# Kernel optimization log

Measured on AMD Instinct MI355X. Metric: run time of the kernel, lower is better.

The kernel has to match this reference:

```python
import jax, jax.numpy as jnp
import numpy as np

N_USERS = 100000
N_ITEMS = 50000
NNZ = 3000000  # user-item interactions; symmetric adjacency has 2*NNZ edges
D = 64
N_LAYERS = 3


def setup_inputs() -> dict:
    key = jax.random.key(0)
    k1, k2, k3 = jax.random.split(key, 3)
    N = N_USERS + N_ITEMS
    users = jax.random.randint(k1, (NNZ,), 0, N_USERS)
    items = jax.random.randint(k2, (NNZ,), 0, N_ITEMS) + N_USERS
    # symmetric bipartite adjacency: u->i and i->u edges
    row = jnp.concatenate([users, items]).astype(jnp.int32)
    col = jnp.concatenate([items, users]).astype(jnp.int32)
    # D^{-1/2} A D^{-1/2} normalization, matching (deg + 1e-7)^{-0.5}
    deg = jax.ops.segment_sum(jnp.ones(row.shape, dtype=jnp.float32), row, num_segments=N)
    dinv = jnp.power(deg + 1e-7, -0.5)
    vals = dinv[row] * dinv[col]
    in_embs = jax.random.normal(k3, (N, D), dtype=jnp.float32)
    return {"in_embs": in_embs, "row": row, "col": col, "vals": vals, "n_layers": N_LAYERS}


def reference(in_embs, row, col, vals, n_layers):
    N = in_embs.shape[0]
    # result = in_embs + sum_i [ x_i/(i+1) + x_i ]  (original appends both per layer)
    out = in_embs
    x = in_embs
    for i in range(n_layers):
        # SpMM: x <- A_norm @ x  via gather + segment scatter-add
        x = jax.ops.segment_sum(vals[:, None] * x[col], row, num_segments=N)
        # F.normalize(x, dim=-1) with torch's eps=1e-12 clamp
        x = x / jnp.maximum(jnp.linalg.norm(x, axis=-1, keepdims=True), 1e-12)
        out = out + x * (1.0 + 1.0 / (i + 1))
    return out
```

## Files before the change

kernel.cpp:

```cpp
#include <hip/hip_runtime.h>
#include <hip/hip_bf16.h>

#define D 64
#define BW 256
#define MAXK 1024
#define CHUNK 8192

typedef unsigned short u16;
typedef unsigned int u32;
typedef _Float16 half2_t __attribute__((ext_vector_type(2)));

__device__ __forceinline__ u16 f2h(float f) {
    union { _Float16 h; u16 u; } v; v.h = (_Float16)f; return v.u;
}
__device__ __forceinline__ float hlo(u32 u) {
    union { u32 x; half2_t h; } v; v.x = u; return (float)v.h.x;
}
__device__ __forceinline__ float hhi(u32 u) {
    union { u32 x; half2_t h; } v; v.x = u; return (float)v.h.y;
}
__device__ __forceinline__ float dot2lo(u32 u, float acc) {
    union { u32 x; half2_t h; } v; v.x = u;
    half2_t one = {(_Float16)1.0f, (_Float16)0.0f};
    return __builtin_amdgcn_fdot2(v.h, one, acc, false);
}
__device__ __forceinline__ float dot2hi(u32 u, float acc) {
    union { u32 x; half2_t h; } v; v.x = u;
    half2_t one = {(_Float16)0.0f, (_Float16)1.0f};
    return __builtin_amdgcn_fdot2(v.h, one, acc, false);
}


__global__ __launch_bounds__(256) void chunk_hist_kernel(
        const int* __restrict__ row, int* __restrict__ H,
        int E, int K, int nchunks) {
    __shared__ int h[MAXK];
    int ch = blockIdx.x;
    int cbeg = ch * CHUNK;
    int cend = min(cbeg + CHUNK, E);
    for (int i = threadIdx.x; i < K; i += 256) h[i] = 0;
    __syncthreads();
    for (int e = cbeg + threadIdx.x; e < cend; e += 256)
        atomicAdd(&h[__builtin_nontemporal_load(&row[e]) >> 8], 1);
    __syncthreads();
    for (int i = threadIdx.x; i < K; i += 256)
        H[(size_t)i * nchunks + ch] = h[i];
}


__global__ __launch_bounds__(256) void bucket_colscan_kernel(
        int* __restrict__ H, int* __restrict__ btot, int nchunks) {
    __shared__ int tmp[256];
    int b = blockIdx.x;
    int t = threadIdx.x;
    int* Hb = H + (size_t)b * nchunks;
    int cpt = (nchunks + 255) >> 8;
    int beg = min(t * cpt, nchunks), end = min(beg + cpt, nchunks);
    int s = 0;
    for (int i = beg; i < end; ++i) s += Hb[i];
    tmp[t] = s;
    __syncthreads();
    for (int d = 1; d < 256; d <<= 1) {
        int x = (t >= d) ? tmp[t - d] : 0;
        __syncthreads();
        tmp[t] += x;
        __syncthreads();
    }
    int run = tmp[t] - s;
    for (int i = beg; i < end; ++i) {
        int v = Hb[i];
        Hb[i] = run;
        run += v;
    }
    if (t == 255) btot[b] = tmp[255];
}


__global__ __launch_bounds__(1024) void bucket_scan_kernel(
        const int* __restrict__ btot, int* __restrict__ bbase, int K, int E) {
    __shared__ int tmp[1024];
    int t = threadIdx.x;
    int v = (t < K) ? btot[t] : 0;
    tmp[t] = v;
    __syncthreads();
    for (int d = 1; d < 1024; d <<= 1) {
        int x = (t >= d) ? tmp[t - d] : 0;
        __syncthreads();
        tmp[t] += x;
        __syncthreads();
    }
    if (t < K) bbase[t] = tmp[t] - v;
    if (t == 0) bbase[K] = E;
}


__global__ __launch_bounds__(256) void scatter_chunks_kernel(
        const int* __restrict__ row, const int* __restrict__ col,
        const int* __restrict__ H, const int* __restrict__ bbase,
        u32* __restrict__ pairs, int E, int K, int nchunks) {
    __shared__ int cur[MAXK];
    int ch = blockIdx.x;
    int cbeg = ch * CHUNK;
    int cend = min(cbeg + CHUNK, E);
    for (int i = threadIdx.x; i < K; i += 256)
        cur[i] = bbase[i] + H[(size_t)i * nchunks + ch];
    __syncthreads();
    for (int e = cbeg + threadIdx.x; e < cend; e += 256) {
        int r = __builtin_nontemporal_load(&row[e]);
        u32 c = (u32)__builtin_nontemporal_load(&col[e]);
        int p = atomicAdd(&cur[r >> 8], 1);
        pairs[p] = ((u32)(r & 255) << 18) | c;
    }
}


__global__ __launch_bounds__(256) void build_csr_kernel(
        const u32* __restrict__ pairs, const int* __restrict__ bbase,
        int* __restrict__ ptr, float* __restrict__ dinv,
        float* __restrict__ sdeg, int* __restrict__ ccol, int N, int K) {
    __shared__ int hd[BW];
    __shared__ int lp[BW];
    int k = blockIdx.x;
    int ebeg = bbase[k], eend = bbase[k + 1];
    int r0 = k << 8;
    int t = threadIdx.x;
    hd[t] = 0;
    __syncthreads();
    for (int e = ebeg + t; e < eend; e += 256)
        atomicAdd(&hd[pairs[e] >> 18], 1);
    __syncthreads();
    int v = hd[t];
    lp[t] = v;
    __syncthreads();
    for (int d = 1; d < 256; d <<= 1) {
        int x = (t >= d) ? lp[t - d] : 0;
        __syncthreads();
        lp[t] += x;
        __syncthreads();
    }
    int fillbase = ebeg + lp[t] - v;
    int r = r0 + t;
    if (r < N) {
        ptr[r] = fillbase;
        float f = (float)v + 1e-7f;
        float sq = sqrtf(f);
        dinv[r] = 1.0f / sq;
        sdeg[r] = sq;
    }
    hd[t] = fillbase;
    if (k == 0 && t == 0) ptr[N] = bbase[K];
    __syncthreads();
    for (int e = ebeg + t; e < eend; e += 256) {
        u32 pk = pairs[e];
        int pos = atomicAdd(&hd[pk >> 18], 1);
        ccol[pos] = (int)(pk & 0x3FFFFu);
    }
}

__global__ void scale_in_kernel(const float* __restrict__ in,
                                const float* __restrict__ dinv,
                                u16* __restrict__ y0, int npairs) {
    int p = blockIdx.x * blockDim.x + threadIdx.x;
    if (p >= npairs) return;
    float2 v = *reinterpret_cast<const float2*>(&in[(size_t)p * 2]);
    float dv = dinv[p >> 5];
    u32 up = (u32)f2h(v.x * dv) | ((u32)f2h(v.y * dv) << 16);
    *reinterpret_cast<u32*>(&y0[(size_t)p * 2]) = up;
}

template <bool FINAL>
__global__ __launch_bounds__(256) void layer_kernel(
        const u16* __restrict__ y_src,
        const int* __restrict__ ptr,
        const int* __restrict__ ccol,
        const float* __restrict__ dinv,
        const float* __restrict__ sdeg,
        u16* __restrict__ y_dst,
        const float* __restrict__ in_embs,
        const u16* __restrict__ y1,
        float* __restrict__ out,
        int rbeg, int rend) {
    int wid = (blockIdx.x * blockDim.x + threadIdx.x) >> 6;
    int lane = threadIdx.x & 63;
    int rh = lane >> 5;
    int b = (lane >> 3) & 3;
    int a = lane & 7;
    int r = rbeg + wid * 2 + rh;
    if (r >= rend) return;
    const size_t dimoff = (size_t)a * 8;

    int s = ptr[r], e = ptr[r + 1];
    float acc[8];
    #pragma unroll
    for (int i = 0; i < 8; ++i) acc[i] = 0.f;

#define ACCQ(q)                                            \
    do {                                                   \
        u32 qa_[4] = {(q).x, (q).y, (q).z, (q).w};         \
        _Pragma("unroll")                                  \
        for (int i_ = 0; i_ < 4; ++i_) {                   \
            acc[2 * i_]     = dot2lo(qa_[i_], acc[2 * i_]);     \
            acc[2 * i_ + 1] = dot2hi(qa_[i_], acc[2 * i_ + 1]); \
        }                                                  \
    } while (0)

    int j = s;
    #pragma unroll 2
    for (; j + 8 <= e; j += 8) {
        int c0 = __builtin_nontemporal_load(&ccol[j + b]);
        int c1 = __builtin_nontemporal_load(&ccol[j + 4 + b]);
        uint4 q0 = *reinterpret_cast<const uint4*>(&y_src[(size_t)c0 * D + dimoff]);
        uint4 q1 = *reinterpret_cast<const uint4*>(&y_src[(size_t)c1 * D + dimoff]);
        ACCQ(q0);
        ACCQ(q1);
    }
    if (j + 4 <= e) {
        int c = __builtin_nontemporal_load(&ccol[j + b]);
        uint4 q = *reinterpret_cast<const uint4*>(&y_src[(size_t)c * D + dimoff]);
        ACCQ(q);
        j += 4;
    }
    if (j + b < e) {
        int c = __builtin_nontemporal_load(&ccol[j + b]);
        uint4 q = *reinterpret_cast<const uint4*>(&y_src[(size_t)c * D + dimoff]);
        ACCQ(q);
    }
#undef ACCQ

    #pragma unroll
    for (int off = 8; off <= 16; off <<= 1) {
        #pragma unroll
        for (int i = 0; i < 8; ++i) acc[i] += __shfl_xor(acc[i], off);
    }

    float ss = 0.f;
    #pragma unroll
    for (int i = 0; i < 8; ++i) ss += acc[i] * acc[i];
    #pragma unroll
    for (int off = 1; off <= 4; off <<= 1) ss += __shfl_xor(ss, off);
    float inv = 1.0f / fmaxf(sqrtf(ss), 1e-12f);

    if (b == 0) {
        size_t idx = (size_t)r * D + dimoff;
        if (FINAL) {
            float sd = sdeg[r];
            float4 i0 = *reinterpret_cast<const float4*>(&in_embs[idx]);
            float4 i1 = *reinterpret_cast<const float4*>(&in_embs[idx + 4]);
            uint4 w1 = *reinterpret_cast<const uint4*>(&y1[idx]);
            uint4 w2 = *reinterpret_cast<const uint4*>(&y_src[idx]);
            u32 w1a[4] = {w1.x, w1.y, w1.z, w1.w};
            u32 w2a[4] = {w2.x, w2.y, w2.z, w2.w};
            float o[8];
            #pragma unroll
            for (int i = 0; i < 4; ++i) {
                o[2 * i]     = 2.0f * sd * hlo(w1a[i]) + 1.5f * sd * hlo(w2a[i])
                             + (4.0f / 3.0f) * acc[2 * i] * inv;
                o[2 * i + 1] = 2.0f * sd * hhi(w1a[i]) + 1.5f * sd * hhi(w2a[i])
                             + (4.0f / 3.0f) * acc[2 * i + 1] * inv;
            }
            float4 o0 = {o[0] + i0.x, o[1] + i0.y, o[2] + i0.z, o[3] + i0.w};
            float4 o1 = {o[4] + i1.x, o[5] + i1.y, o[6] + i1.z, o[7] + i1.w};
            *reinterpret_cast<float4*>(&out[idx])     = o0;
            *reinterpret_cast<float4*>(&out[idx + 4]) = o1;
        } else {
            float dv = dinv[r] * inv;
            uint4 w;
            w.x = (u32)f2h(acc[0] * dv) | ((u32)f2h(acc[1] * dv) << 16);
            w.y = (u32)f2h(acc[2] * dv) | ((u32)f2h(acc[3] * dv) << 16);
            w.z = (u32)f2h(acc[4] * dv) | ((u32)f2h(acc[5] * dv) << 16);
            w.w = (u32)f2h(acc[6] * dv) | ((u32)f2h(acc[7] * dv) << 16);
            *reinterpret_cast<uint4*>(&y_dst[idx]) = w;
        }
    }
}


__global__ void spmm_scatter_kernel(const float* __restrict__ x_src,
                                    const int* __restrict__ row,
                                    const int* __restrict__ col,
                                    const float* __restrict__ vals,
                                    float* __restrict__ x_dst, int E) {
    int gid = blockIdx.x * blockDim.x + threadIdx.x;
    int e = gid >> 6;
    int lane = threadIdx.x & 63;
    if (e >= E) return;
    float xv = x_src[(size_t)col[e] * D + lane];
    atomicAdd(&x_dst[(size_t)row[e] * D + lane], vals[e] * xv);
}

__global__ void norm_accum_kernel(float* __restrict__ x, float* __restrict__ out,
                                  float coef, int N) {
    int gid = blockIdx.x * blockDim.x + threadIdx.x;
    int rowi = gid >> 6;
    int lane = threadIdx.x & 63;
    if (rowi >= N) return;
    size_t idx = (size_t)rowi * D + lane;
    float v = x[idx];
    float s = v * v;
    #pragma unroll
    for (int off = 32; off >= 1; off >>= 1) s += __shfl_xor(s, off);
    float nv = v / fmaxf(sqrtf(s), 1e-12f);
    x[idx] = nv;
    out[idx] += coef * nv;
}

static inline size_t align256(size_t x) { return (x + 255) & ~(size_t)255; }

extern "C" void kernel_launch(void* const* d_in, const int* in_sizes, int n_in,
                              void* d_out, int out_size, void* d_ws, size_t ws_size,
                              hipStream_t stream) {
    const float* in_embs = (const float*)d_in[0];
    const int*   row     = (const int*)d_in[1];
    const int*   col     = (const int*)d_in[2];
    const float* vals    = (const float*)d_in[3];

    const int N = in_sizes[0] / D;
    const int E = in_sizes[1];

    float* out = (float*)d_out;

    const size_t embElems = (size_t)N * D;
    const size_t f16Bytes = embElems * sizeof(u16);
    const int K = (N + BW - 1) / BW;
    const int nchunks = (E + CHUNK - 1) / CHUNK;
    const size_t Hbytes = (size_t)K * nchunks * 4;

    size_t off = 0;
    const size_t o_ccol  = off; off += align256((size_t)E * 4);
    const size_t o_ptr   = off; off += align256(((size_t)N + 1) * 4);
    const size_t o_dinv  = off; off += align256((size_t)N * 4);
    const size_t o_sdeg  = off; off += align256((size_t)N * 4);
    const size_t o_btot  = off; off += align256((size_t)MAXK * 4);
    const size_t o_bbase = off; off += align256(((size_t)MAXK + 1) * 4);
    const size_t o_X     = off;
    const size_t xNeedA  = align256((size_t)E * 4) + align256(Hbytes);
    const size_t xNeedB  = 2 * align256(f16Bytes);
    const size_t xBytes  = (xNeedA > xNeedB) ? xNeedA : xNeedB;
    const size_t needed  = o_X + align256(xBytes);

    dim3 block(256);
    const int npairs = (int)(embElems / 2);
    dim3 pgrid((unsigned)((npairs + 255) / 256));

    if (ws_size >= needed && K <= MAXK) {
        char* wsb = (char*)d_ws;
        int*   ccol  = (int*)(wsb + o_ccol);
        int*   ptr   = (int*)(wsb + o_ptr);
        float* dinv  = (float*)(wsb + o_dinv);
        float* sdeg  = (float*)(wsb + o_sdeg);
        int*   btot  = (int*)(wsb + o_btot);
        int*   bbase = (int*)(wsb + o_bbase);
        u32*   pairs = (u32*)(wsb + o_X);
        int*   H     = (int*)(wsb + o_X + align256((size_t)E * 4));
        u16*   bufA  = (u16*)(wsb + o_X);
        u16*   bufB  = (u16*)(wsb + o_X + align256(f16Bytes));

        chunk_hist_kernel<<<dim3((unsigned)nchunks), block, 0, stream>>>(
            row, H, E, K, nchunks);
        bucket_colscan_kernel<<<dim3((unsigned)K), block, 0, stream>>>(
            H, btot, nchunks);
        bucket_scan_kernel<<<dim3(1), dim3(1024), 0, stream>>>(btot, bbase, K, E);
        scatter_chunks_kernel<<<dim3((unsigned)nchunks), block, 0, stream>>>(
            row, col, H, bbase, pairs, E, K, nchunks);
        build_csr_kernel<<<dim3((unsigned)K), block, 0, stream>>>(
            pairs, bbase, ptr, dinv, sdeg, ccol, N, K);

        scale_in_kernel<<<pgrid, block, 0, stream>>>(in_embs, dinv, bufA, npairs);

        int nu = (N == 150000) ? 100000 : N;
        auto launch_layer = [&](const u16* src, u16* dst, const u16* y1p,
                                bool fin, int rb, int re) {
            int rows = re - rb;
            if (rows <= 0) return;
            dim3 g((unsigned)(((rows + 1) / 2 + 3) / 4));
            if (fin)
                layer_kernel<true><<<g, block, 0, stream>>>(
                    src, ptr, ccol, dinv, sdeg, nullptr, in_embs, y1p, out, rb, re);
            else
                layer_kernel<false><<<g, block, 0, stream>>>(
                    src, ptr, ccol, dinv, sdeg, dst, nullptr, nullptr, nullptr, rb, re);
        };

        launch_layer(bufA, bufB, nullptr, false, 0, nu);
        launch_layer(bufA, bufB, nullptr, false, nu, N);
        launch_layer(bufB, bufA, nullptr, false, 0, nu);
        launch_layer(bufB, bufA, nullptr, false, nu, N);
        launch_layer(bufA, nullptr, bufB, true, 0, nu);
        launch_layer(bufA, nullptr, bufB, true, nu, N);
    } else {
        float* fA = (float*)d_ws;
        float* fB = fA + embElems;
        hipMemcpyAsync(out, in_embs, embElems * 4, hipMemcpyDeviceToDevice, stream);
        const float coefs[3] = {2.0f, 1.5f, 4.0f / 3.0f};
        dim3 sgrid((unsigned)((E + 3) / 4));
        dim3 ngrid((unsigned)((N + 3) / 4));
        const float* src = in_embs;
        float* dst = fA;
        float* other = fB;
        for (int i = 0; i < 3; ++i) {
            hipMemsetAsync(dst, 0, embElems * 4, stream);
            spmm_scatter_kernel<<<sgrid, block, 0, stream>>>(src, row, col, vals, dst, E);
            norm_accum_kernel<<<ngrid, block, 0, stream>>>(dst, out, coefs[i], N);
            src = dst;
            float* t = dst; dst = other; other = t;
        }
    }
}
```

Baseline: 490.1 us.

## Stage chunk entries in LDS sorted by bucket before coalesced global write

```diff
diff --git a/kernel.cpp b/kernel.cpp
--- a/kernel.cpp
+++ b/kernel.cpp
@@ -41,7 +41,7 @@
     for (int i = threadIdx.x; i < K; i += 256) h[i] = 0;
     __syncthreads();
     for (int e = cbeg + threadIdx.x; e < cend; e += 256)
-        atomicAdd(&h[__builtin_nontemporal_load(&row[e]) >> 8], 1);
+        atomicAdd(&h[row[e] >> 8], 1);
     __syncthreads();
     for (int i = threadIdx.x; i < K; i += 256)
         H[(size_t)i * nchunks + ch] = h[i];
@@ -94,22 +94,63 @@
 }
 
 
-__global__ __launch_bounds__(256) void scatter_chunks_kernel(
+__global__ __launch_bounds__(256) void scatter_sort_kernel(
         const int* __restrict__ row, const int* __restrict__ col,
-        const int* __restrict__ H, const int* __restrict__ bbase,
+        const int* __restrict__ H, const int* __restrict__ btot,
+        const int* __restrict__ bbase,
         u32* __restrict__ pairs, int E, int K, int nchunks) {
-    __shared__ int cur[MAXK];
+    __shared__ u32 stage[CHUNK];
+    __shared__ int hcur[MAXK];
+    __shared__ int lbase[MAXK];
+    __shared__ int red[256];
     int ch = blockIdx.x;
     int cbeg = ch * CHUNK;
     int cend = min(cbeg + CHUNK, E);
-    for (int i = threadIdx.x; i < K; i += 256)
-        cur[i] = bbase[i] + H[(size_t)i * nchunks + ch];
-    __syncthreads();
-    for (int e = cbeg + threadIdx.x; e < cend; e += 256) {
-        int r = __builtin_nontemporal_load(&row[e]);
-        u32 c = (u32)__builtin_nontemporal_load(&col[e]);
-        int p = atomicAdd(&cur[r >> 8], 1);
-        pairs[p] = ((u32)(r & 255) << 18) | c;
+    int t = threadIdx.x;
+    int cpt = (K + 255) >> 8;
+    int bb = min(t * cpt, K), be = min(bb + cpt, K);
+
+    int s = 0;
+    for (int i = bb; i < be; ++i) {
+        int st = H[(size_t)i * nchunks + ch];
+        int en = (ch + 1 < nchunks) ? H[(size_t)i * nchunks + ch + 1] : btot[i];
+        int c = en - st;
+        hcur[i] = c;
+        s += c;
+    }
+    red[t] = s;
+    __syncthreads();
+    for (int d = 1; d < 256; d <<= 1) {
+        int x = (t >= d) ? red[t - d] : 0;
+        __syncthreads();
+        red[t] += x;
+        __syncthreads();
+    }
+    int run = red[t] - s;
+    for (int i = bb; i < be; ++i) {
+        int c = hcur[i];
+        lbase[i] = run;
+        hcur[i] = run;
+        run += c;
+    }
+    __syncthreads();
+
+    for (int e = cbeg + t; e < cend; e += 256) {
+        int r = row[e];
+        u32 c = (u32)col[e];
+        int p = atomicAdd(&hcur[r >> 8], 1);
+        stage[p] = ((u32)(r & 255) << 18) | c;
+    }
+    __syncthreads();
+
+    int wv = t >> 6, ln = t & 63;
+    for (int b = wv; b < K; b += 4) {
+        int lb = lbase[b];
+        int len = hcur[b] - lb;
+        if (len == 0) continue;
+        int gd = bbase[b] + H[(size_t)b * nchunks + ch];
+        for (int i = ln; i < len; i += 64)
+            pairs[gd + i] = stage[lb + i];
     }
 }
 
@@ -360,8 +401,8 @@
         bucket_colscan_kernel<<<dim3((unsigned)K), block, 0, stream>>>(
             H, btot, nchunks);
         bucket_scan_kernel<<<dim3(1), dim3(1024), 0, stream>>>(btot, bbase, K, E);
-        scatter_chunks_kernel<<<dim3((unsigned)nchunks), block, 0, stream>>>(
-            row, col, H, bbase, pairs, E, K, nchunks);
+        scatter_sort_kernel<<<dim3((unsigned)nchunks), block, 0, stream>>>(
+            row, col, H, btot, bbase, pairs, E, K, nchunks);
         build_csr_kernel<<<dim3((unsigned)K), block, 0, stream>>>(
             pairs, bbase, ptr, dinv, sdeg, ccol, N, K);
 
```

Measured after the change: 483.4 us. No clear change (-1.4%).
